# Optimization experiments

Hardware: AMD Instinct MI355X
Metric: run time of the kernel (lower is better)

Reference implementation:

```python
import jax, jax.numpy as jnp
import numpy as np

P, G, F, H = 128, 256, 1024, 512
EPS = 1e-5

def _bn(x, g, b, m, v):
    # eval-mode BatchNorm1d over last dim
    return (x - m) / jnp.sqrt(v + EPS) * g + b

def _lrelu(x):
    return jnp.where(x > 0, x, 0.1 * x)

def setup_inputs():
    key = jax.random.key(0)
    ks = iter(jax.random.split(key, 64))
    rn = lambda s, sc=1.0: jax.random.normal(next(ks), s, dtype=jnp.float32) * sc
    ru = lambda s: jax.random.uniform(next(ks), s, dtype=jnp.float32) + 0.5
    return {
        "f_p": rn((P, F)), "f_g": rn((G, F)),
        "bn_g": ru((F,)), "bn_b": rn((F,), 0.1), "bn_m": rn((F,), 0.1), "bn_v": ru((F,)),
        "rf_W1": rn((F, F), 0.02), "rf_b1": rn((F,), 0.01),
        "rf1_g": ru((F,)), "rf1_b": rn((F,), 0.1), "rf1_m": rn((F,), 0.1), "rf1_v": ru((F,)),
        "rf_W2": rn((F, F), 0.02), "rf_b2": rn((F,), 0.01),
        "rf2_g": ru((F,)), "rf2_b": rn((F,), 0.1), "rf2_m": rn((F,), 0.1), "rf2_v": ru((F,)),
        "sfc_W": rn((F, H), 0.02), "sfc_b": rn((H,), 0.01),
        "sbn_g": ru((H,)), "sbn_b": rn((H,), 0.1), "sbn_m": rn((H,), 0.1), "sbn_v": ru((H,)),
        "scl_W": rn((H, 1), 0.001), "scl_b": rn((1,), 0.001),
        "ffc_W": rn((F, H), 0.02), "ffc_b": rn((H,), 0.01),
        "fbn_g": ru((H,)), "fbn_b": rn((H,), 0.1), "fbn_m": rn((H,), 0.1), "fbn_v": ru((H,)),
        "cls_W": rn((H, 1), 0.001), "cls_b": rn((1,), 0.001),
    }

def reference(f_p, f_g, bn_g, bn_b, bn_m, bn_v,
              rf_W1, rf_b1, rf1_g, rf1_b, rf1_m, rf1_v,
              rf_W2, rf_b2, rf2_g, rf2_b, rf2_m, rf2_v,
              sfc_W, sfc_b, sbn_g, sbn_b, sbn_m, sbn_v, scl_W, scl_b,
              ffc_W, ffc_b, fbn_g, fbn_b, fbn_m, fbn_v, cls_W, cls_b):
    # Siamese difference feature for every probe-gallery pair: d [P,G,F]
    d = _bn((f_p[:, None, :] - f_g[None, :, :]) ** 2, bn_g, bn_b, bn_m, bn_v)
    h = _lrelu(_bn(d @ rf_W1 + rf_b1, rf1_g, rf1_b, rf1_m, rf1_v))
    t = _lrelu(_bn(h @ rf_W2 + rf_b2, rf2_g, rf2_b, rf2_m, rf2_v))
    # Gallery-gallery scalar affinities via Siamese FcBlock + ClassBlock: w [G,G]
    dg = _bn((f_g[:, None, :] - f_g[None, :, :]) ** 2, bn_g, bn_b, bn_m, bn_v)
    hg = _lrelu(_bn(dg @ sfc_W + sfc_b, sbn_g, sbn_b, sbn_m, sbn_v))
    w = (hg @ scl_W + scl_b)[..., 0]
    # Graph diffusion over the gallery axis: d_new = t @ w  [P,G,F]
    d_new = jnp.einsum('pgf,gh->phf', t, w)
    # Per-pair FC + classifier -> scalar score per (probe, gallery) pair
    feat = _lrelu(_bn(d_new @ ffc_W + ffc_b, fbn_g, fbn_b, fbn_m, fbn_v))
    result = (feat @ cls_W + cls_b)[..., 0]
    return result
```

## Files before the change

kernel.cpp:

```cpp
#include <hip/hip_runtime.h>


typedef __bf16 bf16;
typedef __attribute__((ext_vector_type(8))) __bf16 bf16x8;
typedef __attribute__((ext_vector_type(4))) float f32x4;

#define EPSV 1e-5f

__device__ __forceinline__ void async_load16(const bf16* g, bf16* l) {
    __builtin_amdgcn_global_load_lds(
        (const __attribute__((address_space(1))) void*)g,
        (__attribute__((address_space(3))) void*)l, 16, 0, 0);
}

__global__ __launch_bounds__(256) void prep_kernel(
    const float* __restrict__ g, const float* __restrict__ b,
    const float* __restrict__ m, const float* __restrict__ v,
    const float* __restrict__ bias, float* __restrict__ scale,
    float* __restrict__ offset, int n)
{
    int i = blockIdx.x * 256 + threadIdx.x;
    if (i >= n) return;
    float s = g[i] / sqrtf(v[i] + EPSV);
    float o = b[i] - m[i] * s;
    if (bias) o += bias[i] * s;
    scale[i] = s;
    offset[i] = o;
}

__global__ __launch_bounds__(256) void wtrans_kernel(
    const float* __restrict__ in, bf16* __restrict__ out, int K, int N)
{
    int k = blockIdx.x * 256 + threadIdx.x;
    int n = blockIdx.y;
    out[(size_t)n * K + k] = (bf16)in[(size_t)k * N + n];
}

__global__ __launch_bounds__(256) void wconv_kernel(
    const float* __restrict__ w_acc, const float* __restrict__ sclb,
    bf16* __restrict__ wT)
{
    int tid = blockIdx.x * 256 + threadIdx.x;
    int g2 = tid >> 8, g1 = tid & 255;
    int idx = ((g1 >> 4) <= (g2 >> 4)) ? (g1 * 256 + g2) : (g2 * 256 + g1);
    wT[tid] = (bf16)(w_acc[idx] + sclb[0]);
}

__global__ __launch_bounds__(256) void finout_kernel(
    const float* __restrict__ acc, const float* __restrict__ clsb,
    float* __restrict__ out)
{
    int i = blockIdx.x * 256 + threadIdx.x;
    out[i] = acc[i] + clsb[0];
}

__global__ __launch_bounds__(256) void dprep_kernel(
    const float* __restrict__ X, const float* __restrict__ Y,
    const float* __restrict__ ps, const float* __restrict__ po,
    bf16* __restrict__ d, int rowOff)
{
    int t  = blockIdx.x * 256 + threadIdx.x;
    int k0 = (t & 127) * 8;
    int r  = t >> 7;
    int gr = rowOff + r;
    const float* xp = X + (size_t)(gr >> 8) * 1024 + k0;
    const float* yp = Y + (size_t)(gr & 255) * 1024 + k0;
    f32x4 x0 = *(const f32x4*)xp, x1 = *(const f32x4*)(xp + 4);
    f32x4 y0 = *(const f32x4*)yp, y1 = *(const f32x4*)(yp + 4);
    f32x4 sa = *(const f32x4*)(ps + k0), sb = *(const f32x4*)(ps + k0 + 4);
    f32x4 oa = *(const f32x4*)(po + k0), ob = *(const f32x4*)(po + k0 + 4);
    bf16x8 dv;
#pragma unroll
    for (int j = 0; j < 4; ++j) {
        float d0 = x0[j] - y0[j];
        float d1 = x1[j] - y1[j];
        dv[j]     = (bf16)(d0 * d0 * sa[j] + oa[j]);
        dv[j + 4] = (bf16)(d1 * d1 * sb[j] + ob[j]);
    }
    *(bf16x8*)&d[(size_t)r * 1024 + k0] = dv;
}

__global__ __launch_bounds__(512) void gemm256(
    const bf16* __restrict__ A,
    const bf16* __restrict__ BT,
    bf16* __restrict__ C,
    int K, int N,
    long long batchA, long long batchB, long long batchC,
    const float* __restrict__ scale, const float* __restrict__ offset,
    int lrelu,
    const float* __restrict__ fuseW, float* __restrict__ facc,
    long long faccStride)
{
    __shared__ bf16 As[2 * 256 * 64];
    __shared__ bf16 Bs[2 * 256 * 64];
    const int tid  = threadIdx.x;
    const int lane = tid & 63;
    const int wave = tid >> 6;
    const int wrow = wave >> 2, wcol = wave & 3;
    const int q = lane >> 4, l16 = lane & 15;
    const int z = blockIdx.z;

    int bx = blockIdx.x, by = blockIdx.y;
    {
        int nwg = gridDim.x * gridDim.y;
        if (gridDim.z == 1 && (nwg & 7) == 0) {
            int lin = by * gridDim.x + bx;
            int cpx = nwg >> 3;
            int s = (lin & 7) * cpx + (lin >> 3);
            bx = s % gridDim.x;
            by = s / gridDim.x;
        }
    }
    const int row0 = by * 256;
    const int col0 = bx * 256;

    const bf16* Ap = A + (size_t)z * (size_t)batchA;
    const bf16* Bp = BT + (size_t)z * (size_t)batchB;

    f32x4 acc[8][4];
#pragma unroll
    for (int mi = 0; mi < 8; ++mi)
#pragma unroll
        for (int ni = 0; ni < 4; ++ni)
#pragma unroll
            for (int e = 0; e < 4; ++e) acc[mi][ni][e] = 0.f;

    auto stageA = [&](int kk, bf16* dst) {
#pragma unroll
        for (int t = 0; t < 4; ++t) {
            int idx = t * 512 + tid;
            int r = idx >> 3, sch = idx & 7;
            int gch = sch ^ (r & 7);
            async_load16(Ap + (size_t)(row0 + r) * K + kk + gch * 8,
                         &dst[idx * 8]);
        }
    };
    auto stageB = [&](int kk, bf16* dst) {
#pragma unroll
        for (int t = 0; t < 4; ++t) {
            int idx = t * 512 + tid;
            int r = idx >> 3, sch = idx & 7;
            int gch = sch ^ (r & 7);
            async_load16(Bp + (size_t)(col0 + r) * K + kk + gch * 8,
                         &dst[idx * 8]);
        }
    };

    stageA(0, As);
    stageB(0, Bs);

    int cur = 0;
    const int nt = K >> 6;
    for (int t = 0; t < nt; ++t) {
        const bool pf = (t + 1) < nt;
        if (pf) {
            stageA(t * 64 + 64, As + (cur ^ 1) * 16384);
            stageB(t * 64 + 64, Bs + (cur ^ 1) * 16384);
        }
        if (pf) {
            asm volatile("s_waitcnt vmcnt(8)\n\ts_barrier" ::: "memory");
        } else {
            asm volatile("s_waitcnt vmcnt(0) lgkmcnt(0)\n\ts_barrier"
                         ::: "memory");
        }

        const bf16* Asb = As + cur * 16384;
        const bf16* Bsb = Bs + cur * 16384;
#pragma unroll
        for (int s = 0; s < 2; ++s) {
            bf16x8 af[8], bfr[4];
#pragma unroll
            for (int mi = 0; mi < 8; ++mi) {
                int r = wrow * 128 + mi * 16 + l16;
                af[mi] = *(const bf16x8*)&Asb[r * 64 + (((s * 4 + q) ^ (r & 7)) * 8)];
            }
#pragma unroll
            for (int ni = 0; ni < 4; ++ni) {
                int rc = wcol * 64 + ni * 16 + l16;
                bfr[ni] = *(const bf16x8*)&Bsb[rc * 64 + (((s * 4 + q) ^ (rc & 7)) * 8)];
            }
#pragma unroll
            for (int mi = 0; mi < 8; ++mi)
#pragma unroll
                for (int ni = 0; ni < 4; ++ni)
                    acc[mi][ni] = __builtin_amdgcn_mfma_f32_16x16x32_bf16(
                        af[mi], bfr[ni], acc[mi][ni], 0, 0, 0);
        }
        if (pf) asm volatile("s_barrier" ::: "memory");
        cur ^= 1;
    }

    if (fuseW) {
#pragma unroll
        for (int mi = 0; mi < 8; ++mi)
#pragma unroll
            for (int i = 0; i < 4; ++i) {
                float rs = 0.f;
#pragma unroll
                for (int ni = 0; ni < 4; ++ni) {
                    int cc = col0 + wcol * 64 + ni * 16 + l16;
                    float val = acc[mi][ni][i] * scale[cc] + offset[cc];
                    val = val > 0.f ? val : 0.1f * val;
                    rs += val * fuseW[cc];
                }
                rs += __shfl_xor(rs, 1, 64);
                rs += __shfl_xor(rs, 2, 64);
                rs += __shfl_xor(rs, 4, 64);
                rs += __shfl_xor(rs, 8, 64);
                if (l16 == 0) {
                    int r = row0 + wrow * 128 + mi * 16 + q * 4 + i;
                    atomicAdd(facc + (size_t)z * faccStride + r, rs);
                }
            }
        return;
    }
    bf16* Cp = C + (size_t)z * (size_t)batchC;
#pragma unroll
    for (int mi = 0; mi < 8; ++mi)
#pragma unroll
        for (int ni = 0; ni < 4; ++ni)
#pragma unroll
            for (int i = 0; i < 4; ++i) {
                int r = row0 + wrow * 128 + mi * 16 + q * 4 + i;
                int cc = col0 + wcol * 64 + ni * 16 + l16;
                float val = acc[mi][ni][i];
                if (scale) val = val * scale[cc] + offset[cc];
                if (lrelu) val = val > 0.f ? val : 0.1f * val;
                Cp[(size_t)r * N + cc] = (bf16)val;
            }
}

__global__ __launch_bounds__(512) void gemm_aff(
    const float* __restrict__ pairX,
    const float* __restrict__ ps, const float* __restrict__ po,
    const bf16* __restrict__ BT,
    int K,
    const float* __restrict__ scale, const float* __restrict__ offset,
    const float* __restrict__ sclW, float* __restrict__ w_acc)
{
    __shared__ bf16 As[256 * 64];
    __shared__ bf16 Bs[128 * 64];
    const int tid  = threadIdx.x;
    const int lane = tid & 63;
    const int wave = tid >> 6;
    const int wrow = wave >> 1, wcol = wave & 1;
    const int q = lane >> 4, l16 = lane & 15;
    const int col0 = blockIdx.x * 128;

    int ta = 0, rem = blockIdx.y;
    while (rem >= 16 - ta) { rem -= 16 - ta; ++ta; }
    const int tb = ta + rem;

    f32x4 acc[4][4];
#pragma unroll
    for (int mi = 0; mi < 4; ++mi)
#pragma unroll
        for (int ni = 0; ni < 4; ++ni)
#pragma unroll
            for (int e = 0; e < 4; ++e) acc[mi][ni][e] = 0.f;

    for (int kk = 0; kk < K; kk += 64) {
#pragma unroll
        for (int t = 0; t < 4; ++t) {
            int c = tid + t * 512;
            int r = c >> 3, ch = c & 7;
            int g1 = ta * 16 + (r >> 4), g2 = tb * 16 + (r & 15);
            const float* xp = pairX + (size_t)g1 * K + kk + ch * 8;
            const float* yp = pairX + (size_t)g2 * K + kk + ch * 8;
            f32x4 x0 = *(const f32x4*)xp, x1 = *(const f32x4*)(xp + 4);
            f32x4 y0 = *(const f32x4*)yp, y1 = *(const f32x4*)(yp + 4);
            f32x4 sa = *(const f32x4*)(ps + kk + ch * 8);
            f32x4 sb = *(const f32x4*)(ps + kk + ch * 8 + 4);
            f32x4 oa = *(const f32x4*)(po + kk + ch * 8);
            f32x4 ob = *(const f32x4*)(po + kk + ch * 8 + 4);
            bf16x8 dv;
#pragma unroll
            for (int j = 0; j < 4; ++j) {
                float d0 = x0[j] - y0[j];
                float d1 = x1[j] - y1[j];
                dv[j]     = (bf16)(d0 * d0 * sa[j] + oa[j]);
                dv[j + 4] = (bf16)(d1 * d1 * sb[j] + ob[j]);
            }
            *(bf16x8*)&As[r * 64 + ((ch ^ (r & 7)) * 8)] = dv;
        }
#pragma unroll
        for (int t = 0; t < 2; ++t) {
            int idx = t * 512 + tid;
            int r = idx >> 3, sch = idx & 7;
            int gch = sch ^ (r & 7);
            async_load16(BT + (size_t)(col0 + r) * K + kk + gch * 8,
                         &Bs[idx * 8]);
        }
        __syncthreads();

#pragma unroll
        for (int s = 0; s < 2; ++s) {
            bf16x8 af[4], bfr[4];
#pragma unroll
            for (int mi = 0; mi < 4; ++mi) {
                int r = wrow * 64 + mi * 16 + l16;
                af[mi] = *(const bf16x8*)&As[r * 64 + (((s * 4 + q) ^ (r & 7)) * 8)];
            }
#pragma unroll
            for (int ni = 0; ni < 4; ++ni) {
                int rc = wcol * 64 + ni * 16 + l16;
                bfr[ni] = *(const bf16x8*)&Bs[rc * 64 + (((s * 4 + q) ^ (rc & 7)) * 8)];
            }
#pragma unroll
            for (int mi = 0; mi < 4; ++mi)
#pragma unroll
                for (int ni = 0; ni < 4; ++ni)
                    acc[mi][ni] = __builtin_amdgcn_mfma_f32_16x16x32_bf16(
                        af[mi], bfr[ni], acc[mi][ni], 0, 0, 0);
        }
        __syncthreads();
    }

#pragma unroll
    for (int mi = 0; mi < 4; ++mi)
#pragma unroll
        for (int i = 0; i < 4; ++i) {
            float rs = 0.f;
#pragma unroll
            for (int ni = 0; ni < 4; ++ni) {
                int cc = col0 + wcol * 64 + ni * 16 + l16;
                float val = acc[mi][ni][i] * scale[cc] + offset[cc];
                val = val > 0.f ? val : 0.1f * val;
                rs += val * sclW[cc];
            }
            rs += __shfl_xor(rs, 1, 64);
            rs += __shfl_xor(rs, 2, 64);
            rs += __shfl_xor(rs, 4, 64);
            rs += __shfl_xor(rs, 8, 64);
            if (l16 == 0) {
                int r = wrow * 64 + mi * 16 + q * 4 + i;
                int g1 = ta * 16 + (r >> 4), g2 = tb * 16 + (r & 15);
                atomicAdd(w_acc + g1 * 256 + g2, rs);
            }
        }
}

extern "C" void kernel_launch(void* const* d_in, const int* in_sizes, int n_in,
                              void* d_out, int out_size, void* d_ws, size_t ws_size,
                              hipStream_t stream)
{
    const float* f_p   = (const float*)d_in[0];
    const float* f_g   = (const float*)d_in[1];
    const float* bn_g  = (const float*)d_in[2];
    const float* bn_b  = (const float*)d_in[3];
    const float* bn_m  = (const float*)d_in[4];
    const float* bn_v  = (const float*)d_in[5];
    const float* rf_W1 = (const float*)d_in[6];
    const float* rf_b1 = (const float*)d_in[7];
    const float* rf1_g = (const float*)d_in[8];
    const float* rf1_b = (const float*)d_in[9];
    const float* rf1_m = (const float*)d_in[10];
    const float* rf1_v = (const float*)d_in[11];
    const float* rf_W2 = (const float*)d_in[12];
    const float* rf_b2 = (const float*)d_in[13];
    const float* rf2_g = (const float*)d_in[14];
    const float* rf2_b = (const float*)d_in[15];
    const float* rf2_m = (const float*)d_in[16];
    const float* rf2_v = (const float*)d_in[17];
    const float* sfc_W = (const float*)d_in[18];
    const float* sfc_b = (const float*)d_in[19];
    const float* sbn_g = (const float*)d_in[20];
    const float* sbn_b = (const float*)d_in[21];
    const float* sbn_m = (const float*)d_in[22];
    const float* sbn_v = (const float*)d_in[23];
    const float* scl_W = (const float*)d_in[24];
    const float* scl_b = (const float*)d_in[25];
    const float* ffc_W = (const float*)d_in[26];
    const float* ffc_b = (const float*)d_in[27];
    const float* fbn_g = (const float*)d_in[28];
    const float* fbn_b = (const float*)d_in[29];
    const float* fbn_m = (const float*)d_in[30];
    const float* fbn_v = (const float*)d_in[31];
    const float* cls_W = (const float*)d_in[32];
    const float* cls_b = (const float*)d_in[33];

    const size_t MB = 1ull << 20;
    char* ws = (char*)d_ws;
    float* SC      = (float*)(ws);
    float *s0 = SC,        *o0 = SC + 1024;
    float *s1 = SC + 2048, *o1 = SC + 3072;
    float *s2 = SC + 4096, *o2 = SC + 5120;
    float *s3 = SC + 6144, *o3 = SC + 6656;
    float *s4 = SC + 7168, *o4 = SC + 7680;
    float* w_acc   = (float*)(ws + 65536);
    float* out_acc = (float*)(ws + 327680);
    bf16* wT       = (bf16*)(ws + 458752);
    bf16* W1T      = (bf16*)(ws + 1 * MB);
    bf16* W2T      = (bf16*)(ws + 3 * MB);
    bf16* sfcT     = (bf16*)(ws + 5 * MB);
    bf16* ffcT     = (bf16*)(ws + 6 * MB);

    int nc;
    if      (ws_size >= 170 * MB) nc = 1;
    else if (ws_size >= 90 * MB)  nc = 2;
    else                          nc = 4;
    const int pc = 128 / nc;
    const int R  = pc * 256;
    const size_t hbytes = (size_t)R * 1024 * 2;
    bf16* bufA = (bf16*)(ws + 8 * MB);
    bf16* bufB = (bf16*)(ws + 8 * MB + hbytes);
    bf16* bufC = (bf16*)(ws + 8 * MB + 2 * hbytes);

    prep_kernel<<<dim3(4), 256, 0, stream>>>(bn_g, bn_b, bn_m, bn_v, nullptr, s0, o0, 1024);
    prep_kernel<<<dim3(4), 256, 0, stream>>>(rf1_g, rf1_b, rf1_m, rf1_v, rf_b1, s1, o1, 1024);
    prep_kernel<<<dim3(4), 256, 0, stream>>>(rf2_g, rf2_b, rf2_m, rf2_v, rf_b2, s2, o2, 1024);
    prep_kernel<<<dim3(2), 256, 0, stream>>>(sbn_g, sbn_b, sbn_m, sbn_v, sfc_b, s3, o3, 512);
    prep_kernel<<<dim3(2), 256, 0, stream>>>(fbn_g, fbn_b, fbn_m, fbn_v, ffc_b, s4, o4, 512);

    wtrans_kernel<<<dim3(4, 1024), 256, 0, stream>>>(rf_W1, W1T, 1024, 1024);
    wtrans_kernel<<<dim3(4, 1024), 256, 0, stream>>>(rf_W2, W2T, 1024, 1024);
    wtrans_kernel<<<dim3(4, 512), 256, 0, stream>>>(sfc_W, sfcT, 1024, 512);
    wtrans_kernel<<<dim3(4, 512), 256, 0, stream>>>(ffc_W, ffcT, 1024, 512);

    hipMemsetAsync(ws + 65536, 0, 393216, stream);

    gemm_aff<<<dim3(4, 136), 512, 0, stream>>>(
        f_g, s0, o0, sfcT, 1024, s3, o3, scl_W, w_acc);
    wconv_kernel<<<dim3(256), 256, 0, stream>>>(w_acc, scl_b, wT);

    for (int ci = 0; ci < nc; ++ci) {
        dprep_kernel<<<dim3(R / 2), 256, 0, stream>>>(
            f_p, f_g, s0, o0, bufB, ci * R);
        gemm256<<<dim3(4, R / 256), 512, 0, stream>>>(
            bufB, W1T, bufA, 1024, 1024,
            0, 0, 0, s1, o1, 1, nullptr, nullptr, 0);
        gemm256<<<dim3(4, R / 256), 512, 0, stream>>>(
            bufA, W2T, bufB, 1024, 1024,
            0, 0, 0, s2, o2, 1, nullptr, nullptr, 0);
        gemm256<<<dim3(1, 2, pc), 512, 0, stream>>>(
            ffcT, bufB, bufC, 1024, 256,
            0, (long long)256 * 1024, (long long)512 * 256,
            nullptr, nullptr, 0, nullptr, nullptr, 0);
        gemm256<<<dim3(2, 1, pc), 512, 0, stream>>>(
            wT, bufC, nullptr, 256, 512,
            0, (long long)512 * 256, 0,
            s4, o4, 1, cls_W, out_acc + (size_t)ci * pc * 256, 256);
    }
    finout_kernel<<<dim3(128), 256, 0, stream>>>(out_acc, cls_b, (float*)d_out);
}
```

Before: 547.7 us.

## Split GEMM k-tile into four phases with finer-grained async staging and setprio

New measurement: 520.9 us. -4.9%, faster.

```diff
diff --git a/kernel.cpp b/kernel.cpp
--- a/kernel.cpp
+++ b/kernel.cpp
@@ -80,6 +80,35 @@
     *(bf16x8*)&d[(size_t)r * 1024 + k0] = dv;
 }
 
+#define PHASE(ASB, BSB, Q, READB, STAGE_STMT, VM_STMT)                        \
+  {                                                                           \
+    if (READB) {                                                              \
+      _Pragma("unroll") for (int ni = 0; ni < 4; ++ni) {                      \
+        int rc = wcol * 64 + ni * 16 + l16;                                   \
+        bfr[ni][0] = *(const bf16x8*)&(BSB)[rc * 64 + (((q) ^ (rc & 7)) * 8)];\
+        bfr[ni][1] = *(const bf16x8*)&(BSB)[rc * 64 + (((4 + q) ^ (rc & 7)) * 8)];\
+      }                                                                       \
+    }                                                                         \
+    bf16x8 afq[2][2];                                                         \
+    _Pragma("unroll") for (int m2 = 0; m2 < 2; ++m2) {                        \
+      int r = wrow * 128 + ((Q) * 2 + m2) * 16 + l16;                         \
+      afq[m2][0] = *(const bf16x8*)&(ASB)[r * 64 + (((q) ^ (r & 7)) * 8)];    \
+      afq[m2][1] = *(const bf16x8*)&(ASB)[r * 64 + (((4 + q) ^ (r & 7)) * 8)];\
+    }                                                                         \
+    STAGE_STMT;                                                               \
+    VM_STMT;                                                                  \
+    __builtin_amdgcn_s_barrier();                                             \
+    asm volatile("s_waitcnt lgkmcnt(0)" ::: "memory");                        \
+    __builtin_amdgcn_s_setprio(1);                                            \
+    _Pragma("unroll") for (int s = 0; s < 2; ++s)                             \
+      _Pragma("unroll") for (int m2 = 0; m2 < 2; ++m2)                        \
+        _Pragma("unroll") for (int ni = 0; ni < 4; ++ni)                      \
+          acc[(Q) * 2 + m2][ni] = __builtin_amdgcn_mfma_f32_16x16x32_bf16(    \
+              afq[m2][s], bfr[ni][s], acc[(Q) * 2 + m2][ni], 0, 0, 0);        \
+    __builtin_amdgcn_s_setprio(0);                                            \
+    __builtin_amdgcn_s_barrier();                                             \
+  }
+
 __global__ __launch_bounds__(512) void gemm256(
     const bf16* __restrict__ A,
     const bf16* __restrict__ BT,
@@ -125,69 +154,55 @@
 #pragma unroll
             for (int e = 0; e < 4; ++e) acc[mi][ni][e] = 0.f;
 
-    auto stageA = [&](int kk, bf16* dst) {
-#pragma unroll
-        for (int t = 0; t < 4; ++t) {
-            int idx = t * 512 + tid;
+    auto stageA2 = [&](int kk, int buf, int h) {
+#pragma unroll
+        for (int tt = 0; tt < 2; ++tt) {
+            int idx = (2 * h + tt) * 512 + tid;
             int r = idx >> 3, sch = idx & 7;
             int gch = sch ^ (r & 7);
             async_load16(Ap + (size_t)(row0 + r) * K + kk + gch * 8,
-                         &dst[idx * 8]);
+                         &As[buf * 16384 + idx * 8]);
         }
     };
-    auto stageB = [&](int kk, bf16* dst) {
-#pragma unroll
-        for (int t = 0; t < 4; ++t) {
-            int idx = t * 512 + tid;
+    auto stageB2 = [&](int kk, int buf, int h) {
+#pragma unroll
+        for (int tt = 0; tt < 2; ++tt) {
+            int idx = (2 * h + tt) * 512 + tid;
             int r = idx >> 3, sch = idx & 7;
             int gch = sch ^ (r & 7);
             async_load16(Bp + (size_t)(col0 + r) * K + kk + gch * 8,
-                         &dst[idx * 8]);
+                         &Bs[buf * 16384 + idx * 8]);
         }
     };
 
-    stageA(0, As);
-    stageB(0, Bs);
-
-    int cur = 0;
+    stageA2(0, 0, 0); stageA2(0, 0, 1);
+    stageB2(0, 0, 0); stageB2(0, 0, 1);
+    stageB2(64, 1, 0); stageB2(64, 1, 1);
+    asm volatile("s_waitcnt vmcnt(4)" ::: "memory");
+    __builtin_amdgcn_s_barrier();
+
+    bf16x8 bfr[4][2];
+    const bf16* A0 = As;          const bf16* B0 = Bs;
+    const bf16* A1 = As + 16384;  const bf16* B1 = Bs + 16384;
     const int nt = K >> 6;
-    for (int t = 0; t < nt; ++t) {
-        const bool pf = (t + 1) < nt;
-        if (pf) {
-            stageA(t * 64 + 64, As + (cur ^ 1) * 16384);
-            stageB(t * 64 + 64, Bs + (cur ^ 1) * 16384);
-        }
-        if (pf) {
-            asm volatile("s_waitcnt vmcnt(8)\n\ts_barrier" ::: "memory");
-        } else {
-            asm volatile("s_waitcnt vmcnt(0) lgkmcnt(0)\n\ts_barrier"
-                         ::: "memory");
-        }
-
-        const bf16* Asb = As + cur * 16384;
-        const bf16* Bsb = Bs + cur * 16384;
-#pragma unroll
-        for (int s = 0; s < 2; ++s) {
-            bf16x8 af[8], bfr[4];
-#pragma unroll
-            for (int mi = 0; mi < 8; ++mi) {
-                int r = wrow * 128 + mi * 16 + l16;
-                af[mi] = *(const bf16x8*)&Asb[r * 64 + (((s * 4 + q) ^ (r & 7)) * 8)];
-            }
-#pragma unroll
-            for (int ni = 0; ni < 4; ++ni) {
-                int rc = wcol * 64 + ni * 16 + l16;
-                bfr[ni] = *(const bf16x8*)&Bsb[rc * 64 + (((s * 4 + q) ^ (rc & 7)) * 8)];
-            }
-#pragma unroll
-            for (int mi = 0; mi < 8; ++mi)
-#pragma unroll
-                for (int ni = 0; ni < 4; ++ni)
-                    acc[mi][ni] = __builtin_amdgcn_mfma_f32_16x16x32_bf16(
-                        af[mi], bfr[ni], acc[mi][ni], 0, 0, 0);
-        }
-        if (pf) asm volatile("s_barrier" ::: "memory");
-        cur ^= 1;
+    for (int i2 = 0; i2 < nt; i2 += 2) {
+        const int kk1 = (i2 + 1) << 6, kk2 = (i2 + 2) << 6,
+                  kk3 = (i2 + 3) << 6;
+        const bool more = (i2 + 2) < nt;
+        PHASE(A0, B0, 0, true,  { stageA2(kk1, 1, 0); }, {});
+        PHASE(A0, B0, 1, false, { stageA2(kk1, 1, 1); }, {});
+        PHASE(A0, B0, 2, false, { if (more) stageB2(kk2, 0, 0); }, {});
+        PHASE(A0, B0, 3, false, { if (more) stageB2(kk2, 0, 1); },
+              { if (more)
+                    asm volatile("s_waitcnt vmcnt(4)" ::: "memory");
+                else
+                    asm volatile("s_waitcnt vmcnt(0)" ::: "memory"); });
+        PHASE(A1, B1, 0, true,  { if (more) stageA2(kk2, 0, 0); }, {});
+        PHASE(A1, B1, 1, false, { if (more) stageA2(kk2, 0, 1); }, {});
+        PHASE(A1, B1, 2, false, { if (more) stageB2(kk3, 1, 0); }, {});
+        PHASE(A1, B1, 3, false, { if (more) stageB2(kk3, 1, 1); },
+              { if (more)
+                    asm volatile("s_waitcnt vmcnt(4)" ::: "memory"); });
     }
 
     if (fuseW) {
```
